# Kernel tuning notes

Measured on AMD Instinct MI355X. Metric: run time of the kernel, lower is better.

## Reference

```python
import jax, jax.numpy as jnp
import numpy as np

H = 4          # hidden_size
NUM_LAYERS = 5
SEQ = 610
BATCH = 128


def _lstm_layer(x, w_i, w_h, bi, bh):
    # x: [B, T, I]; w_i: [4H, I]; w_h: [4H, H]; bi, bh: [4H]
    # PyTorch gate order: i, f, g, o
    B = x.shape[0]
    b = bi + bh

    def step(carry, xt):
        h, c = carry
        gates = xt @ w_i.T + h @ w_h.T + b          # [B, 4H]
        i, f, g, o = jnp.split(gates, 4, axis=-1)
        c = jax.nn.sigmoid(f) * c + jax.nn.sigmoid(i) * jnp.tanh(g)
        h = jax.nn.sigmoid(o) * jnp.tanh(c)
        return (h, c), h

    h0 = jnp.zeros((B, H), x.dtype)
    c0 = jnp.zeros((B, H), x.dtype)
    (_, _), hs = jax.lax.scan(step, (h0, c0), jnp.swapaxes(x, 0, 1))  # hs: [T, B, H]
    return jnp.swapaxes(hs, 0, 1)                   # [B, T, H]


def setup_inputs() -> dict:
    key = jax.random.key(0)
    ks = jax.random.split(key, 10)
    s = 1.0 / np.sqrt(H)  # PyTorch default uniform(-1/sqrt(H), 1/sqrt(H))
    u = lambda k, shape: jax.random.uniform(k, shape, jnp.float32, -s, s)
    return {
        "x": jax.random.normal(ks[0], (BATCH, SEQ, 2), jnp.float32),
        "w_ih0": u(ks[1], (4 * H, 2)),
        "w_ih": u(ks[2], (NUM_LAYERS - 1, 4 * H, H)),
        "w_hh": u(ks[3], (NUM_LAYERS, 4 * H, H)),
        "b_ih": u(ks[4], (NUM_LAYERS, 4 * H)),
        "b_hh": u(ks[5], (NUM_LAYERS, 4 * H)),
        "w_lin": u(ks[6], (1, H)),
        "b_lin": u(ks[7], (1,)),
        "w_fc": jax.random.uniform(ks[8], (5, SEQ), jnp.float32, -1.0 / np.sqrt(SEQ), 1.0 / np.sqrt(SEQ)),
        "b_fc": jax.random.uniform(ks[9], (5,), jnp.float32, -1.0 / np.sqrt(SEQ), 1.0 / np.sqrt(SEQ)),
    }


def reference(x, w_ih0, w_ih, w_hh, b_ih, b_hh, w_lin, b_lin, w_fc, b_fc):
    # 5-layer stacked LSTM, zero initial state (as on the module's first call)
    out = _lstm_layer(x, w_ih0, w_hh[0], b_ih[0], b_hh[0])
    for l in range(NUM_LAYERS - 1):
        out = _lstm_layer(out, w_ih[l], w_hh[l + 1], b_ih[l + 1], b_hh[l + 1])
    # per-timestep Linear(4 -> 1) then cat along dim 1 -> [B, T]
    t = (out @ w_lin.T + b_lin)[..., 0]             # [B, 610]
    return t @ w_fc.T + b_fc                         # [B, 5]
```

## Files before the change

### kernel.cpp

```cpp
#include <hip/hip_runtime.h>
#include <math.h>

#define H 4
#define NL 5
#define SEQ 610
#define BATCH 128
#define NITER 619
#define HEAD 16
#define TAIL0 616

typedef float v2f __attribute__((ext_vector_type(2)));

#if __has_builtin(__builtin_elementwise_fma)
#define FMA2(a, b, c) __builtin_elementwise_fma((a), (b), (c))
#else
static __device__ __forceinline__ v2f FMA2(v2f a, v2f b, v2f c) {
    v2f r; r[0] = fmaf(a[0], b[0], c[0]); r[1] = fmaf(a[1], b[1], c[1]); return r;
}
#endif
static __device__ __forceinline__ v2f splat2(float a) { v2f r; r[0] = a; r[1] = a; return r; }

template<int CTRL, int RM, int BM, bool BC>
__device__ __forceinline__ float dppm(float old_, float src) {
    return __int_as_float(__builtin_amdgcn_update_dpp(
        __float_as_int(old_), __float_as_int(src), CTRL, RM, BM, BC));
}

__global__ __launch_bounds__(64) void lstm_jk_kernel(
    const float* __restrict__ x,
    const float* __restrict__ w_ih0,
    const float* __restrict__ w_ih,
    const float* __restrict__ w_hh,
    const float* __restrict__ b_ih,
    const float* __restrict__ b_hh,
    const float* __restrict__ w_lin,
    const float* __restrict__ b_lin,
    const float* __restrict__ w_fc,
    const float* __restrict__ b_fc,
    float* __restrict__ out)
{
    __shared__ float lds_x[SEQ * 2 + 32];
    __shared__ float lds_wfcp[4 * SEQ * 2 + 8];

    const int lane  = threadIdx.x;
    const int l_raw = lane >> 3;
    const int l     = l_raw > 4 ? 4 : l_raw;
    const int j2    = (lane >> 2) & 1;
    const int k     = lane & 3;
    const bool is_l0 = (l_raw == 0);
    const int b     = blockIdx.x;

    {
        const float4* src = (const float4*)(x + (size_t)b * (SEQ * 2));
        float4* dst = (float4*)lds_x;
        for (int i = lane; i < (SEQ * 2) / 4; i += 64) dst[i] = src[i];
    }
    #pragma unroll
    for (int kk = 0; kk < 4; ++kk) {
        for (int t = lane; t < SEQ; t += 64) {
            lds_wfcp[(kk * SEQ + t) * 2 + 0] = w_fc[kk * SEQ + t];
            lds_wfcp[(kk * SEQ + t) * 2 + 1] = w_fc[4 * SEQ + t];
        }
    }
    __syncthreads();

    v2f wip[4], whp[4], bp;
    {
        const int ga = 2 * j2, gb = 2 * j2 + 1;
        const float sa = (ga == 2) ? 2.8853900817779268f : -1.4426950408889634f;
        const float sb = -1.4426950408889634f;
        const int ra = ga * H + k, rb = gb * H + k;
        #pragma unroll
        for (int m = 0; m < 4; ++m) {
            float wa, wb;
            if (l == 0) {
                wa = (m < 2) ? w_ih0[ra * 2 + m] : 0.f;
                wb = (m < 2) ? w_ih0[rb * 2 + m] : 0.f;
            } else {
                wa = w_ih[((l - 1) * 16 + ra) * 4 + m];
                wb = w_ih[((l - 1) * 16 + rb) * 4 + m];
            }
            wip[m][0] = wa * sa; wip[m][1] = wb * sb;
            whp[m][0] = w_hh[(l * 16 + ra) * 4 + m] * sa;
            whp[m][1] = w_hh[(l * 16 + rb) * 4 + m] * sb;
        }
        bp[0] = (b_ih[l * 16 + ra] + b_hh[l * 16 + ra]) * sa;
        bp[1] = (b_ih[l * 16 + rb] + b_hh[l * 16 + rb]) * sb;
    }
    const float wl0 = w_lin[0], wl1 = w_lin[1], wl2 = w_lin[2], wl3 = w_lin[3];
    const float bl  = b_lin[0];
    const int wpbase = k * SEQ;

    float c = 0.f;
    float q0 = 0.f, q1 = 0.f, q2 = 0.f, q3 = 0.f;
    v2f acc2 = splat2(0.f);
    v2f pre;
    {
        const float2 xv0 = *(const float2*)&lds_x[0];
        const float xs0 = is_l0 ? xv0.x : 0.f;
        const float xs1 = is_l0 ? xv0.y : 0.f;
        pre = FMA2(wip[1], splat2(xs1), FMA2(wip[0], splat2(xs0), bp));
    }

    #define TICK_CORE(tau_, GATED, NXv, WVv)                                          \
    {                                                                                 \
        const float oq0 = q0, oq1 = q1, oq2 = q2, oq3 = q3;                           \
                               \
        v2f G = FMA2(whp[3], splat2(oq3), FMA2(whp[2], splat2(oq2),                   \
                FMA2(whp[1], splat2(oq1), FMA2(whp[0], splat2(oq0), pre))));          \
        v2f E; E[0] = __builtin_amdgcn_exp2f(G[0]);                                   \
        E[1] = __builtin_amdgcn_exp2f(G[1]);                                          \
        v2f A = E + 1.f;                            \
        v2f X, Y;                              \
        X[0] = dppm<0x114, 0xF, 0xA, false>(A[0], A[0]);                              \
        X[1] = dppm<0x114, 0xF, 0xA, false>(A[1], A[1]);                              \
        Y[0] = dppm<0x104, 0xF, 0x5, false>(A[0], A[0]);                              \
        Y[1] = dppm<0x104, 0xF, 0x5, false>(A[1], A[1]);                              \
        const float M   = X[0] * Y[0];                                                \
        const float den = M * X[1];                                                   \
        const float num = fmaf(c, M, X[1] * (Y[0] - 2.f));                            \
        float cn = num * __builtin_amdgcn_rcpf(den);                                  \
        if (GATED) { const unsigned tt = (unsigned)((tau_) - 2 * l_raw);              \
                     cn = (tt < SEQ) ? cn : 0.f; }                                    \
        c = cn;                                                                       \
        const float Dc = 1.f + __builtin_amdgcn_exp2f(c * 2.8853900817779268f);       \
        const float hv = (Dc - 2.f) * __builtin_amdgcn_rcpf(Y[1] * Dc);               \
        q0 = dppm<0x00, 0xF, 0xF, true>(0.f, hv);                                     \
        q1 = dppm<0x55, 0xF, 0xF, true>(0.f, hv);                                     \
        q2 = dppm<0xAA, 0xF, 0xF, true>(0.f, hv);                                     \
        q3 = dppm<0xFF, 0xF, 0xF, true>(0.f, hv);                                     \
                  \
        float p0 = dppm<0x118, 0xF, 0xF, true>(0.f, oq0);                             \
        p0 = dppm<0x142, 0x2, 0x3, false>(p0, oq0);                                   \
        p0 = dppm<0x143, 0x4, 0x3, false>(p0, oq0);                                   \
        float p1 = dppm<0x118, 0xF, 0xF, true>(0.f, oq1);                             \
        p1 = dppm<0x142, 0x2, 0x3, false>(p1, oq1);                                   \
        p1 = dppm<0x143, 0x4, 0x3, false>(p1, oq1);                                   \
        float p2 = dppm<0x118, 0xF, 0xF, true>(0.f, oq2);                             \
        p2 = dppm<0x142, 0x2, 0x3, false>(p2, oq2);                                   \
        p2 = dppm<0x143, 0x4, 0x3, false>(p2, oq2);                                   \
        float p3 = dppm<0x118, 0xF, 0xF, true>(0.f, oq3);                             \
        p3 = dppm<0x142, 0x2, 0x3, false>(p3, oq3);                                   \
        p3 = dppm<0x143, 0x4, 0x3, false>(p3, oq3);                                   \
        const float xs0 = is_l0 ? (NXv).x : p0;                                       \
        const float xs1 = is_l0 ? (NXv).y : p1;                                       \
        pre = FMA2(wip[3], splat2(p3), FMA2(wip[2], splat2(p2),                       \
              FMA2(wip[1], splat2(xs1), FMA2(wip[0], splat2(xs0), bp))));             \
        float tval = fmaf(oq0, wl0, fmaf(oq1, wl1, fmaf(oq2, wl2, fmaf(oq3, wl3, bl)))); \
        if (GATED) tval = ((unsigned)((tau_) - 9) < SEQ) ? tval : 0.f;                \
        v2f wvv; wvv[0] = (WVv).x; wvv[1] = (WVv).y;                                  \
        acc2 = FMA2(splat2(tval), wvv, acc2);                                         \
    }

    for (int tau = 0; tau < HEAD; ++tau) {
        const float2 nx = *(const float2*)&lds_x[(tau + 1) * 2];
        int t4 = tau - 9; t4 = t4 < 0 ? 0 : t4;
        const float2 wv = *(const float2*)&lds_wfcp[(wpbase + t4) * 2];
        TICK_CORE(tau, true, nx, wv);
    }

    for (int ch = 0; ch < 75; ++ch) {
        const int tau0 = HEAD + ch * 8;
        float2 xc_[8], wc_[8];
        #pragma unroll
        for (int i = 0; i < 8; ++i) {
            xc_[i] = *(const float2*)&lds_x[(tau0 + 1 + i) * 2];
            wc_[i] = *(const float2*)&lds_wfcp[(wpbase + tau0 + i - 9) * 2];
        }
        #pragma unroll
        for (int i = 0; i < 8; ++i) {
            TICK_CORE(tau0 + i, false, xc_[i], wc_[i]);
        }
    }

    for (int tau = TAIL0; tau < NITER; ++tau) {
        const float2 nx = *(const float2*)&lds_x[(tau + 1) * 2];
        const float2 wv = *(const float2*)&lds_wfcp[(wpbase + tau - 9) * 2];
        TICK_CORE(tau, true, nx, wv);
    }
    #undef TICK_CORE

    if (lane >= 32 && lane < 36) {
        out[b * 5 + k] = acc2[0] + b_fc[k];
        if (k == 0) out[b * 5 + 4] = acc2[1] + b_fc[4];
    }
}

extern "C" void kernel_launch(void* const* d_in, const int* in_sizes, int n_in,
                              void* d_out, int out_size, void* d_ws, size_t ws_size,
                              hipStream_t stream)
{
    const float* x     = (const float*)d_in[0];
    const float* w_ih0 = (const float*)d_in[1];
    const float* w_ih  = (const float*)d_in[2];
    const float* w_hh  = (const float*)d_in[3];
    const float* b_ih  = (const float*)d_in[4];
    const float* b_hh  = (const float*)d_in[5];
    const float* w_lin = (const float*)d_in[6];
    const float* b_lin = (const float*)d_in[7];
    const float* w_fc  = (const float*)d_in[8];
    const float* b_fc  = (const float*)d_in[9];
    float* out = (float*)d_out;

    lstm_jk_kernel<<<dim3(BATCH), dim3(64), 0, stream>>>(
        x, w_ih0, w_ih, w_hh, b_ih, b_hh, w_lin, b_lin, w_fc, b_fc, out);
}
```

Baseline: 157.0 us.

## Split LSTM layers across five wavefronts with LDS handoff and per-step barriers

Result: slower. 232.6 us (+48.1%).

```diff
diff --git a/kernel.cpp b/kernel.cpp
--- a/kernel.cpp
+++ b/kernel.cpp
@@ -2,7 +2,6 @@
 #include <math.h>
 
 #define H 4
-#define NL 5
 #define SEQ 610
 #define BATCH 128
 #define NITER 619
@@ -26,7 +25,7 @@
         __float_as_int(old_), __float_as_int(src), CTRL, RM, BM, BC));
 }
 
-__global__ __launch_bounds__(64) void lstm_jk_kernel(
+__global__ __launch_bounds__(320) void lstm_mw_kernel(
     const float* __restrict__ x,
     const float* __restrict__ w_ih0,
     const float* __restrict__ w_ih,
@@ -39,25 +38,28 @@
     const float* __restrict__ b_fc,
     float* __restrict__ out)
 {
-    __shared__ float lds_x[SEQ * 2 + 32];
-    __shared__ float lds_wfcp[4 * SEQ * 2 + 8];
+    __shared__ __align__(16) float lds_x4[(SEQ + 12) * 4];
+    __shared__ __align__(16) float lds_wfcp[4 * SEQ * 2 + 8];
+    __shared__ __align__(16) float lds_h[5][4][64];
 
-    const int lane  = threadIdx.x;
-    const int l_raw = lane >> 3;
-    const int l     = l_raw > 4 ? 4 : l_raw;
-    const int j2    = (lane >> 2) & 1;
-    const int k     = lane & 3;
-    const bool is_l0 = (l_raw == 0);
-    const int b     = blockIdx.x;
+    const int tid  = threadIdx.x;
+    const int w    = tid >> 6;
+    const int lane = tid & 63;
+    const int j2   = (lane >> 2) & 1;
+    const int k    = lane & 3;
+    const int b    = blockIdx.x;
 
-    {
-        const float4* src = (const float4*)(x + (size_t)b * (SEQ * 2));
-        float4* dst = (float4*)lds_x;
-        for (int i = lane; i < (SEQ * 2) / 4; i += 64) dst[i] = src[i];
+    for (int i = tid; i < (SEQ + 12) * 4; i += 320) lds_x4[i] = 0.f;
+    for (int i = tid; i < 5 * 4 * 64; i += 320) ((float*)lds_h)[i] = 0.f;
+    __syncthreads();
+    for (int t = tid; t < SEQ; t += 320) {
+        const float2 xv = *(const float2*)&x[(size_t)b * (SEQ * 2) + t * 2];
+        lds_x4[t * 4 + 0] = xv.x;
+        lds_x4[t * 4 + 1] = xv.y;
     }
     #pragma unroll
     for (int kk = 0; kk < 4; ++kk) {
-        for (int t = lane; t < SEQ; t += 64) {
+        for (int t = tid; t < SEQ; t += 320) {
             lds_wfcp[(kk * SEQ + t) * 2 + 0] = w_fc[kk * SEQ + t];
             lds_wfcp[(kk * SEQ + t) * 2 + 1] = w_fc[4 * SEQ + t];
         }
@@ -66,121 +68,98 @@
 
     v2f wip[4], whp[4], bp;
     {
-        const int ga = 2 * j2, gb = 2 * j2 + 1;
-        const float sa = (ga == 2) ? 2.8853900817779268f : -1.4426950408889634f;
+        const int ga = 2 * j2, gb = ga + 1;
+        const float sa = (ga == 2) ? 2.8853900817779268f
+                                   : -1.4426950408889634f;
         const float sb = -1.4426950408889634f;
         const int ra = ga * H + k, rb = gb * H + k;
         #pragma unroll
         for (int m = 0; m < 4; ++m) {
             float wa, wb;
-            if (l == 0) {
+            if (w == 0) {
                 wa = (m < 2) ? w_ih0[ra * 2 + m] : 0.f;
                 wb = (m < 2) ? w_ih0[rb * 2 + m] : 0.f;
             } else {
-                wa = w_ih[((l - 1) * 16 + ra) * 4 + m];
-                wb = w_ih[((l - 1) * 16 + rb) * 4 + m];
+                wa = w_ih[((w - 1) * 16 + ra) * 4 + m];
+                wb = w_ih[((w - 1) * 16 + rb) * 4 + m];
             }
             wip[m][0] = wa * sa; wip[m][1] = wb * sb;
-            whp[m][0] = w_hh[(l * 16 + ra) * 4 + m] * sa;
-            whp[m][1] = w_hh[(l * 16 + rb) * 4 + m] * sb;
+            whp[m][0] = w_hh[(w * 16 + ra) * 4 + m] * sa;
+            whp[m][1] = w_hh[(w * 16 + rb) * 4 + m] * sb;
         }
-        bp[0] = (b_ih[l * 16 + ra] + b_hh[l * 16 + ra]) * sa;
-        bp[1] = (b_ih[l * 16 + rb] + b_hh[l * 16 + rb]) * sb;
+        bp[0] = (b_ih[w * 16 + ra] + b_hh[w * 16 + ra]) * sa;
+        bp[1] = (b_ih[w * 16 + rb] + b_hh[w * 16 + rb]) * sb;
     }
     const float wl0 = w_lin[0], wl1 = w_lin[1], wl2 = w_lin[2], wl3 = w_lin[3];
     const float bl  = b_lin[0];
     const int wpbase = k * SEQ;
+
+    #define XIN_PTR(tau_) ((w == 0) ? (const float4*)&lds_x4[((tau_) + 1) * 4] \
+                                    : (const float4*)&lds_h[w - 1][((tau_) + 3) & 3][0])
 
     float c = 0.f;
     float q0 = 0.f, q1 = 0.f, q2 = 0.f, q3 = 0.f;
     v2f acc2 = splat2(0.f);
     v2f pre;
     {
-        const float2 xv0 = *(const float2*)&lds_x[0];
-        const float xs0 = is_l0 ? xv0.x : 0.f;
-        const float xs1 = is_l0 ? xv0.y : 0.f;
+        float xs0 = 0.f, xs1 = 0.f;
+        if (w == 0) { xs0 = lds_x4[0]; xs1 = lds_x4[1]; }
         pre = FMA2(wip[1], splat2(xs1), FMA2(wip[0], splat2(xs0), bp));
     }
 
-    #define TICK_CORE(tau_, GATED, NXv, WVv)                                          \
+    #define TICK(tau_, GATED)                                                         \
     {                                                                                 \
+                          \
+        const float4 xn = *XIN_PTR(tau_);                                             \
+        int t4 = (tau_) - 9;                                                          \
+        if (GATED) t4 = t4 < 0 ? 0 : t4;                                              \
+        const float2 wv = *(const float2*)&lds_wfcp[(wpbase + t4) * 2];               \
         const float oq0 = q0, oq1 = q1, oq2 = q2, oq3 = q3;                           \
-                               \
+                                      \
         v2f G = FMA2(whp[3], splat2(oq3), FMA2(whp[2], splat2(oq2),                   \
                 FMA2(whp[1], splat2(oq1), FMA2(whp[0], splat2(oq0), pre))));          \
-        v2f E; E[0] = __builtin_amdgcn_exp2f(G[0]);                                   \
-        E[1] = __builtin_amdgcn_exp2f(G[1]);                                          \
-        v2f A = E + 1.f;                            \
-        v2f X, Y;                              \
-        X[0] = dppm<0x114, 0xF, 0xA, false>(A[0], A[0]);                              \
-        X[1] = dppm<0x114, 0xF, 0xA, false>(A[1], A[1]);                              \
-        Y[0] = dppm<0x104, 0xF, 0x5, false>(A[0], A[0]);                              \
-        Y[1] = dppm<0x104, 0xF, 0x5, false>(A[1], A[1]);                              \
-        const float M   = X[0] * Y[0];                                                \
-        const float den = M * X[1];                                                   \
-        const float num = fmaf(c, M, X[1] * (Y[0] - 2.f));                            \
+        v2f A; A[0] = 1.f + __builtin_amdgcn_exp2f(G[0]);                             \
+        A[1] = 1.f + __builtin_amdgcn_exp2f(G[1]);                                    \
+        float X0, X1, Y0, Y1;                  \
+        X0 = dppm<0x114, 0xF, 0xA, false>(A[0], A[0]);                                \
+        X1 = dppm<0x114, 0xF, 0xA, false>(A[1], A[1]);                                \
+        Y0 = dppm<0x104, 0xF, 0x5, false>(A[0], A[0]);                                \
+        Y1 = dppm<0x104, 0xF, 0x5, false>(A[1], A[1]);                                \
+        const float M   = X0 * Y0;                                                    \
+        const float den = M * X1;                                                     \
+        const float num = fmaf(c, M, X1 * (Y0 - 2.f));                                \
         float cn = num * __builtin_amdgcn_rcpf(den);                                  \
-        if (GATED) { const unsigned tt = (unsigned)((tau_) - 2 * l_raw);              \
+        if (GATED) { const unsigned tt = (unsigned)((tau_) - 2 * w);                  \
                      cn = (tt < SEQ) ? cn : 0.f; }                                    \
         c = cn;                                                                       \
         const float Dc = 1.f + __builtin_amdgcn_exp2f(c * 2.8853900817779268f);       \
-        const float hv = (Dc - 2.f) * __builtin_amdgcn_rcpf(Y[1] * Dc);               \
+        const float hv = (Dc - 2.f) * __builtin_amdgcn_rcpf(Y1 * Dc);                 \
+                 \
+        lds_h[w][(tau_) & 3][lane] = hv;                                              \
+                                             \
         q0 = dppm<0x00, 0xF, 0xF, true>(0.f, hv);                                     \
         q1 = dppm<0x55, 0xF, 0xF, true>(0.f, hv);                                     \
         q2 = dppm<0xAA, 0xF, 0xF, true>(0.f, hv);                                     \
         q3 = dppm<0xFF, 0xF, 0xF, true>(0.f, hv);                                     \
-                  \
-        float p0 = dppm<0x118, 0xF, 0xF, true>(0.f, oq0);                             \
-        p0 = dppm<0x142, 0x2, 0x3, false>(p0, oq0);                                   \
-        p0 = dppm<0x143, 0x4, 0x3, false>(p0, oq0);                                   \
-        float p1 = dppm<0x118, 0xF, 0xF, true>(0.f, oq1);                             \
-        p1 = dppm<0x142, 0x2, 0x3, false>(p1, oq1);                                   \
-        p1 = dppm<0x143, 0x4, 0x3, false>(p1, oq1);                                   \
-        float p2 = dppm<0x118, 0xF, 0xF, true>(0.f, oq2);                             \
-        p2 = dppm<0x142, 0x2, 0x3, false>(p2, oq2);                                   \
-        p2 = dppm<0x143, 0x4, 0x3, false>(p2, oq2);                                   \
-        float p3 = dppm<0x118, 0xF, 0xF, true>(0.f, oq3);                             \
-        p3 = dppm<0x142, 0x2, 0x3, false>(p3, oq3);                                   \
-        p3 = dppm<0x143, 0x4, 0x3, false>(p3, oq3);                                   \
-        const float xs0 = is_l0 ? (NXv).x : p0;                                       \
-        const float xs1 = is_l0 ? (NXv).y : p1;                                       \
-        pre = FMA2(wip[3], splat2(p3), FMA2(wip[2], splat2(p2),                       \
-              FMA2(wip[1], splat2(xs1), FMA2(wip[0], splat2(xs0), bp))));             \
+                                        \
+        pre = FMA2(wip[3], splat2(xn.w), FMA2(wip[2], splat2(xn.z),                   \
+              FMA2(wip[1], splat2(xn.y), FMA2(wip[0], splat2(xn.x), bp))));           \
+                              \
         float tval = fmaf(oq0, wl0, fmaf(oq1, wl1, fmaf(oq2, wl2, fmaf(oq3, wl3, bl)))); \
         if (GATED) tval = ((unsigned)((tau_) - 9) < SEQ) ? tval : 0.f;                \
-        v2f wvv; wvv[0] = (WVv).x; wvv[1] = (WVv).y;                                  \
+        v2f wvv; wvv[0] = wv.x; wvv[1] = wv.y;                                        \
         acc2 = FMA2(splat2(tval), wvv, acc2);                                         \
+        __syncthreads();                                                              \
     }
 
-    for (int tau = 0; tau < HEAD; ++tau) {
-        const float2 nx = *(const float2*)&lds_x[(tau + 1) * 2];
-        int t4 = tau - 9; t4 = t4 < 0 ? 0 : t4;
-        const float2 wv = *(const float2*)&lds_wfcp[(wpbase + t4) * 2];
-        TICK_CORE(tau, true, nx, wv);
-    }
+    for (int tau = 0; tau < HEAD; ++tau) TICK(tau, true);
+    #pragma unroll 2
+    for (int tau = HEAD; tau < TAIL0; ++tau) TICK(tau, false);
+    for (int tau = TAIL0; tau < NITER; ++tau) TICK(tau, true);
+    #undef TICK
+    #undef XIN_PTR
 
-    for (int ch = 0; ch < 75; ++ch) {
-        const int tau0 = HEAD + ch * 8;
-        float2 xc_[8], wc_[8];
-        #pragma unroll
-        for (int i = 0; i < 8; ++i) {
-            xc_[i] = *(const float2*)&lds_x[(tau0 + 1 + i) * 2];
-            wc_[i] = *(const float2*)&lds_wfcp[(wpbase + tau0 + i - 9) * 2];
-        }
-        #pragma unroll
-        for (int i = 0; i < 8; ++i) {
-            TICK_CORE(tau0 + i, false, xc_[i], wc_[i]);
-        }
-    }
-
-    for (int tau = TAIL0; tau < NITER; ++tau) {
-        const float2 nx = *(const float2*)&lds_x[(tau + 1) * 2];
-        const float2 wv = *(const float2*)&lds_wfcp[(wpbase + tau - 9) * 2];
-        TICK_CORE(tau, true, nx, wv);
-    }
-    #undef TICK_CORE
-
-    if (lane >= 32 && lane < 36) {
+    if (w == 4 && lane < 4) {
         out[b * 5 + k] = acc2[0] + b_fc[k];
         if (k == 0) out[b * 5 + 4] = acc2[1] + b_fc[4];
     }
@@ -202,6 +181,6 @@
     const float* b_fc  = (const float*)d_in[9];
     float* out = (float*)d_out;
 
-    lstm_jk_kernel<<<dim3(BATCH), dim3(64), 0, stream>>>(
+    lstm_mw_kernel<<<dim3(BATCH), dim3(320), 0, stream>>>(
         x, w_ih0, w_ih, w_hh, b_ih, b_hh, w_lin, b_lin, w_fc, b_fc, out);
 }
```
